# Kernel optimization log

Hardware: AMD Instinct MI355X
Metric: run time of the kernel (lower is better)

Reference implementation:

```python
import jax, jax.numpy as jnp
import numpy as np

M, IN_F, OUT_F = 16384, 2048, 2048

def sign_fn(x):
    # torch.sign(torch.sign(x) + 0.5): maps 0 -> +1, otherwise +/-1
    return jnp.sign(jnp.sign(x) + 0.5)

def setup_inputs() -> dict:
    key = jax.random.key(0)
    kx, kw = jax.random.split(key)
    # Upstream BNN activations are binary +/-1 (required for the packed-bit
    # backward in the original module to be exact).
    x = sign_fn(jax.random.normal(kx, (M, IN_F), dtype=jnp.float32))
    weight = jax.random.uniform(kw, (OUT_F, IN_F), dtype=jnp.float32) * 0.01
    return {"x": x, "weight": weight}

def reference(x, weight):
    # xnor=False path: SignFunctionNoSTE -> binarize weight, then dense matmul
    b_weight = sign_fn(weight)          # [OUT_F, IN_F], values in {-1, +1}
    return x @ b_weight.T               # [M, OUT_F]
```

## Files before the change

### kernel.cpp

```cpp
#include <hip/hip_runtime.h>
#include <stdint.h>

typedef unsigned long long u64;

#define M_DIM 16384
#define N_DIM 2048
#define K_DIM 2048

#define BM 256
#define BN 256
#define BK 64
#define NSTAGE (K_DIM / BK)

typedef int v4i  __attribute__((ext_vector_type(4)));
typedef int v16i __attribute__((ext_vector_type(16)));


__device__ __forceinline__ void gld16(void* lds_base, const void* gsrc) {
    __builtin_amdgcn_global_load_lds(
        (const __attribute__((address_space(1))) uint32_t*)gsrc,
        (__attribute__((address_space(3))) uint32_t*)lds_base,
        16, 0, 0);
}

__device__ __forceinline__ int pk4(float a, float b, float c, float d) {
    int r = (a < 0.0f ? 0xFF : 0x01);
    r |= (b < 0.0f ? 0xFF : 0x01) << 8;
    r |= (c < 0.0f ? 0xFF : 0x01) << 16;
    r |= (d < 0.0f ? 0xFF : 0x01) << 24;
    return r;
}

template <int T>
__global__ __launch_bounds__(256) void pack_i8_kernel(
        const float* __restrict__ src, char* __restrict__ dst) {
    const int wave_id = (blockIdx.x * 256 + threadIdx.x) >> 6;
    const int lane = threadIdx.x & 63;
    const int s  = wave_id & (NSTAGE - 1);
    const int rg = wave_id >> 5;
    const int r  = lane & 31;
    const int kh = lane >> 5;
    const int regs = 2 * T;
    char* out = dst + ((size_t)rg * NSTAGE + s) * (regs * 1024) + lane * 16;
#pragma unroll 2
    for (int rr = 0; rr < regs; ++rr) {
        const int c = rr / T, t = rr % T;
        const int row = rg * (T * 32) + t * 32 + r;
        const float* p = src + (size_t)row * K_DIM + s * BK + c * 32 + kh * 16;
        const float4 v0 = ((const float4*)p)[0];
        const float4 v1 = ((const float4*)p)[1];
        const float4 v2 = ((const float4*)p)[2];
        const float4 v3 = ((const float4*)p)[3];
        int4 o;
        o.x = pk4(v0.x, v0.y, v0.z, v0.w);
        o.y = pk4(v1.x, v1.y, v1.z, v1.w);
        o.z = pk4(v2.x, v2.y, v2.z, v2.w);
        o.w = pk4(v3.x, v3.y, v3.z, v3.w);
        *(int4*)(out + rr * 1024) = o;
    }
}

__global__ __launch_bounds__(512, 2) void bgemm_i8_kernel(
        const char* __restrict__ Ap, const char* __restrict__ Bp,
        float* __restrict__ C) {
    __shared__ __align__(16) char lds[2][32 * 1024];

    const int t    = threadIdx.x;
    const int lane = t & 63;
    const int wv   = t >> 6;
    const int wm   = (wv >> 1) & 3;
    const int wn   = wv & 1;

    const int id    = blockIdx.x;
    const int xcd   = id & 7;
    const int idx   = id >> 3;
    const int m_blk = xcd * 8 + (idx & 7);
    const int n_blk = idx >> 3;

    const char* aG = Ap + (size_t)m_blk * (NSTAGE * 16384);
    const char* bG = Bp + (size_t)n_blk * (NSTAGE * 16384);

    v16i acc[2][4];
#pragma unroll
    for (int i = 0; i < 2; ++i)
#pragma unroll
        for (int j = 0; j < 4; ++j)
#pragma unroll
            for (int q = 0; q < 16; ++q) acc[i][j][q] = 0;

    auto dma = [&](int s, int buf) {
        const char* a = aG + (size_t)s * 16384;
        const char* b = bG + (size_t)s * 16384;
#pragma unroll
        for (int r = 0; r < 4; ++r) {
            const int reg = wv * 4 + r;
            const char* g = (reg < 16) ? (a + reg * 1024)
                                       : (b + (reg - 16) * 1024);
            gld16(&lds[buf][reg * 1024], g + lane * 16);
        }
    };

    auto compute = [&](int buf) {
        const char* As = lds[buf];
        const char* Bs = lds[buf] + 16384;
#pragma unroll
        for (int c = 0; c < 2; ++c) {
            v4i af[2], bf[4];
#pragma unroll
            for (int i = 0; i < 2; ++i)
                af[i] = *(const v4i*)(As + (c * 8 + wm * 2 + i) * 1024 + lane * 16);
#pragma unroll
            for (int j = 0; j < 4; ++j)
                bf[j] = *(const v4i*)(Bs + (c * 8 + wn * 4 + j) * 1024 + lane * 16);
#pragma unroll
            for (int i = 0; i < 2; ++i)
#pragma unroll
                for (int j = 0; j < 4; ++j)
                    acc[i][j] = __builtin_amdgcn_mfma_i32_32x32x32_i8(
                        af[i], bf[j], acc[i][j], 0, 0, 0);
        }
    };

    dma(0, 0);
    __syncthreads();
#pragma unroll 1
    for (int s = 0; s < NSTAGE; ++s) {
        if (s + 1 < NSTAGE) dma(s + 1, (s + 1) & 1);
        compute(s & 1);
        __syncthreads();
    }

    const int col = lane & 31;
    const int rq  = (lane >> 5) * 4;
#pragma unroll
    for (int i = 0; i < 2; ++i) {
#pragma unroll
        for (int j = 0; j < 4; ++j) {
            const int mbase = m_blk * BM + (wm * 2 + i) * 32;
            const int nbase = n_blk * BN + (wn * 4 + j) * 32;
#pragma unroll
            for (int q = 0; q < 16; ++q) {
                const int row = mbase + (q & 3) + 8 * (q >> 2) + rq;
                C[(size_t)row * N_DIM + nbase + col] = (float)acc[i][j][q];
            }
        }
    }
}

#define KC 32
#define KT 16
struct alignas(16) u64x2 { u64 x, y; };

__global__ __launch_bounds__(256) void pack_sign_kernel(
        const float* __restrict__ in, u64* __restrict__ out, int ngroups) {
    int wid  = (blockIdx.x * 256 + threadIdx.x) >> 6;
    int lane = threadIdx.x & 63;
    if (wid >= ngroups) return;
    const float4* p = reinterpret_cast<const float4*>(in) + (size_t)wid * 64 + lane;
    float4 v = *p;
    u64 b0 = __ballot(v.x < 0.0f);
    u64 b1 = __ballot(v.y < 0.0f);
    u64 b2 = __ballot(v.z < 0.0f);
    u64 b3 = __ballot(v.w < 0.0f);
    if (lane == 0) {
        u64* o = out + (size_t)wid * 4;
        o[0] = b0; o[1] = b1; o[2] = b2; o[3] = b3;
    }
}

__global__ __launch_bounds__(256, 2) void bgemm_kernel(
        const u64* __restrict__ A, const u64* __restrict__ B,
        float* __restrict__ C) {
    __shared__ u64 As[KT][128];
    __shared__ u64 Bs[KT][128];
    const int t     = threadIdx.x;
    const int m_blk = blockIdx.y << 7;
    const int n_blk = blockIdx.x << 7;
    const int lane = t & 63;
    const int wave = t >> 6;
    const int tm   = lane >> 3;
    const int tn   = lane & 7;
    const int m0   = ((wave >> 1) << 6) + (tm << 3);
    const int n0   = ((wave & 1) << 6) + (tn << 3);
    unsigned acc[8][8];
#pragma unroll
    for (int i = 0; i < 8; ++i)
#pragma unroll
        for (int j = 0; j < 8; ++j) acc[i][j] = 0u;
    const int sr = t >> 3;
    const int sc = (t << 1) & 15;
    for (int ks = 0; ks < K_DIM / (KT * 64); ++ks) {
        const int cbase = ks * KT;
#pragma unroll
        for (int i = 0; i < 4; ++i) {
            int r = i * 32 + sr;
            u64x2 va = *reinterpret_cast<const u64x2*>(A + (size_t)(m_blk + r) * KC + cbase + sc);
            As[sc][r] = va.x; As[sc + 1][r] = va.y;
            u64x2 vb = *reinterpret_cast<const u64x2*>(B + (size_t)(n_blk + r) * KC + cbase + sc);
            Bs[sc][r] = vb.x; Bs[sc + 1][r] = vb.y;
        }
        __syncthreads();
#pragma unroll 1
        for (int c = 0; c < KT; ++c) {
            u64 a[8], b[8];
#pragma unroll
            for (int i = 0; i < 4; ++i) {
                u64x2 va = *reinterpret_cast<const u64x2*>(&As[c][m0 + 2 * i]);
                a[2 * i] = va.x; a[2 * i + 1] = va.y;
                u64x2 vb = *reinterpret_cast<const u64x2*>(&Bs[c][n0 + 2 * i]);
                b[2 * i] = vb.x; b[2 * i + 1] = vb.y;
            }
#pragma unroll
            for (int i = 0; i < 8; ++i)
#pragma unroll
                for (int j = 0; j < 8; ++j)
                    acc[i][j] += (unsigned)__builtin_popcountll(a[i] ^ b[j]);
        }
        __syncthreads();
    }
#pragma unroll
    for (int i = 0; i < 8; ++i) {
        float* o = C + (size_t)(m_blk + m0 + i) * N_DIM + n_blk + n0;
        float4 v0, v1;
        v0.x = (float)(K_DIM - 2 * (int)acc[i][0]);
        v0.y = (float)(K_DIM - 2 * (int)acc[i][1]);
        v0.z = (float)(K_DIM - 2 * (int)acc[i][2]);
        v0.w = (float)(K_DIM - 2 * (int)acc[i][3]);
        v1.x = (float)(K_DIM - 2 * (int)acc[i][4]);
        v1.y = (float)(K_DIM - 2 * (int)acc[i][5]);
        v1.z = (float)(K_DIM - 2 * (int)acc[i][6]);
        v1.w = (float)(K_DIM - 2 * (int)acc[i][7]);
        *reinterpret_cast<float4*>(o)     = v0;
        *reinterpret_cast<float4*>(o + 4) = v1;
    }
}

extern "C" void kernel_launch(void* const* d_in, const int* in_sizes, int n_in,
                              void* d_out, int out_size, void* d_ws, size_t ws_size,
                              hipStream_t stream) {
    const float* x = (const float*)d_in[0];
    const float* w = (const float*)d_in[1];
    float* out = (float*)d_out;

    const size_t needA = (size_t)M_DIM * K_DIM;
    const size_t needB = (size_t)N_DIM * K_DIM;
    if (ws_size >= needA + needB) {
        char* Ap = (char*)d_ws;
        char* Bp = Ap + needA;
        pack_i8_kernel<8><<<2048 / 4, 256, 0, stream>>>(x, Ap);
        pack_i8_kernel<8><<<256 / 4, 256, 0, stream>>>(w, Bp);
        bgemm_i8_kernel<<<(M_DIM / BM) * (N_DIM / BN), 512, 0, stream>>>(Ap, Bp, out);
    } else {
        u64* xb = (u64*)d_ws;
        u64* wb = xb + (size_t)M_DIM * KC;
        int xgroups = (M_DIM * K_DIM) / 256;
        int wgroups = (N_DIM * K_DIM) / 256;
        pack_sign_kernel<<<xgroups / 4, 256, 0, stream>>>(x, xb, xgroups);
        pack_sign_kernel<<<wgroups / 4, 256, 0, stream>>>(w, wb, wgroups);
        bgemm_kernel<<<dim3(N_DIM / 128, M_DIM / 128), 256, 0, stream>>>(xb, wb, out);
    }
}
```

Baseline: 318.8 us.

## Switch binary GEMM from int8 MFMA to FP4 scaled MFMA

Packs the ±1 values as FP4 (E2M1) nibbles (0x2 = +1, 0xA = -1) instead of int8 bytes, halving the packed operand size and the workspace. The GEMM now uses the gfx950 scaled f8f6f4 32x32x64 MFMA with FP4 format and unit scales, covering K=128 per stage and accumulating in fp32. This is meant to cut operand memory traffic and double the K consumed per MFMA. In exchange it depends on the FP4 register layout and operand zero-padding being correct. The fp32 accumulation stays exact because all sums are integers well below 2^24.

Measured after the change: 286.3 us. 10.2% less time.

```diff
diff --git a/kernel.cpp b/kernel.cpp
--- a/kernel.cpp
+++ b/kernel.cpp
@@ -7,14 +7,15 @@
 #define N_DIM 2048
 #define K_DIM 2048
 
+
 #define BM 256
 #define BN 256
-#define BK 64
-#define NSTAGE (K_DIM / BK)
-
-typedef int v4i  __attribute__((ext_vector_type(4)));
-typedef int v16i __attribute__((ext_vector_type(16)));
-
+#define BK 128
+#define NST (K_DIM / BK)
+
+typedef int   v4i  __attribute__((ext_vector_type(4)));
+typedef int   v8i  __attribute__((ext_vector_type(8)));
+typedef float v16f __attribute__((ext_vector_type(16)));
 
 __device__ __forceinline__ void gld16(void* lds_base, const void* gsrc) {
     __builtin_amdgcn_global_load_lds(
@@ -23,44 +24,46 @@
         16, 0, 0);
 }
 
-__device__ __forceinline__ int pk4(float a, float b, float c, float d) {
-    int r = (a < 0.0f ? 0xFF : 0x01);
-    r |= (b < 0.0f ? 0xFF : 0x01) << 8;
-    r |= (c < 0.0f ? 0xFF : 0x01) << 16;
-    r |= (d < 0.0f ? 0xFF : 0x01) << 24;
+__device__ __forceinline__ int pkn(float4 a, float4 b) {
+    int r;
+    r  = (a.x < 0.0f ? 0xA : 0x2);
+    r |= (a.y < 0.0f ? 0xA : 0x2) << 4;
+    r |= (a.z < 0.0f ? 0xA : 0x2) << 8;
+    r |= (a.w < 0.0f ? 0xA : 0x2) << 12;
+    r |= (b.x < 0.0f ? 0xA : 0x2) << 16;
+    r |= (b.y < 0.0f ? 0xA : 0x2) << 20;
+    r |= (b.z < 0.0f ? 0xA : 0x2) << 24;
+    r |= (b.w < 0.0f ? 0xA : 0x2) << 28;
     return r;
 }
 
-template <int T>
-__global__ __launch_bounds__(256) void pack_i8_kernel(
+__global__ __launch_bounds__(256) void pack_fp4_kernel(
         const float* __restrict__ src, char* __restrict__ dst) {
-    const int wave_id = (blockIdx.x * 256 + threadIdx.x) >> 6;
+    const int wid  = (blockIdx.x * 256 + threadIdx.x) >> 6;
     const int lane = threadIdx.x & 63;
-    const int s  = wave_id & (NSTAGE - 1);
-    const int rg = wave_id >> 5;
-    const int r  = lane & 31;
-    const int kh = lane >> 5;
-    const int regs = 2 * T;
-    char* out = dst + ((size_t)rg * NSTAGE + s) * (regs * 1024) + lane * 16;
-#pragma unroll 2
-    for (int rr = 0; rr < regs; ++rr) {
-        const int c = rr / T, t = rr % T;
-        const int row = rg * (T * 32) + t * 32 + r;
-        const float* p = src + (size_t)row * K_DIM + s * BK + c * 32 + kh * 16;
-        const float4 v0 = ((const float4*)p)[0];
-        const float4 v1 = ((const float4*)p)[1];
-        const float4 v2 = ((const float4*)p)[2];
-        const float4 v3 = ((const float4*)p)[3];
-        int4 o;
-        o.x = pk4(v0.x, v0.y, v0.z, v0.w);
-        o.y = pk4(v1.x, v1.y, v1.z, v1.w);
-        o.z = pk4(v2.x, v2.y, v2.z, v2.w);
-        o.w = pk4(v3.x, v3.y, v3.z, v3.w);
-        *(int4*)(out + rr * 1024) = o;
-    }
-}
-
-__global__ __launch_bounds__(512, 2) void bgemm_i8_kernel(
+    const int t    = wid & 7;
+    const int sub  = (wid >> 3) & 1;
+    const int st   = (wid >> 4) & 15;
+    const int blk  = wid >> 8;
+    const int row  = blk * 256 + t * 32 + (lane & 31);
+    const int kb   = st * 128 + sub * 64 + (lane >> 5) * 32;
+    const float4* p = (const float4*)(src + (size_t)row * K_DIM + kb);
+    int4 o;
+    o.x = pkn(p[0], p[1]);
+    o.y = pkn(p[2], p[3]);
+    o.z = pkn(p[4], p[5]);
+    o.w = pkn(p[6], p[7]);
+    *(int4*)(dst + (size_t)wid * 1024 + lane * 16) = o;
+}
+
+__device__ __forceinline__ v8i up8(v4i v) {
+    v8i r;
+    r[0] = v[0]; r[1] = v[1]; r[2] = v[2]; r[3] = v[3];
+    r[4] = 0;    r[5] = 0;    r[6] = 0;    r[7] = 0;
+    return r;
+}
+
+__global__ __launch_bounds__(512, 2) void bgemm_fp4_kernel(
         const char* __restrict__ Ap, const char* __restrict__ Bp,
         float* __restrict__ C) {
     __shared__ __align__(16) char lds[2][32 * 1024];
@@ -77,16 +80,16 @@
     const int m_blk = xcd * 8 + (idx & 7);
     const int n_blk = idx >> 3;
 
-    const char* aG = Ap + (size_t)m_blk * (NSTAGE * 16384);
-    const char* bG = Bp + (size_t)n_blk * (NSTAGE * 16384);
-
-    v16i acc[2][4];
+    const char* aG = Ap + (size_t)m_blk * (NST * 16384);
+    const char* bG = Bp + (size_t)n_blk * (NST * 16384);
+
+    v16f acc[2][4];
 #pragma unroll
     for (int i = 0; i < 2; ++i)
 #pragma unroll
         for (int j = 0; j < 4; ++j)
 #pragma unroll
-            for (int q = 0; q < 16; ++q) acc[i][j][q] = 0;
+            for (int q = 0; q < 16; ++q) acc[i][j][q] = 0.0f;
 
     auto dma = [&](int s, int buf) {
         const char* a = aG + (size_t)s * 16384;
@@ -104,28 +107,31 @@
         const char* As = lds[buf];
         const char* Bs = lds[buf] + 16384;
 #pragma unroll
-        for (int c = 0; c < 2; ++c) {
-            v4i af[2], bf[4];
+        for (int sub = 0; sub < 2; ++sub) {
+            v8i af[2], bf[4];
 #pragma unroll
             for (int i = 0; i < 2; ++i)
-                af[i] = *(const v4i*)(As + (c * 8 + wm * 2 + i) * 1024 + lane * 16);
+                af[i] = up8(*(const v4i*)(As + (sub * 8 + wm * 2 + i) * 1024 + lane * 16));
 #pragma unroll
             for (int j = 0; j < 4; ++j)
-                bf[j] = *(const v4i*)(Bs + (c * 8 + wn * 4 + j) * 1024 + lane * 16);
+                bf[j] = up8(*(const v4i*)(Bs + (sub * 8 + wn * 4 + j) * 1024 + lane * 16));
 #pragma unroll
             for (int i = 0; i < 2; ++i)
 #pragma unroll
                 for (int j = 0; j < 4; ++j)
-                    acc[i][j] = __builtin_amdgcn_mfma_i32_32x32x32_i8(
-                        af[i], bf[j], acc[i][j], 0, 0, 0);
+                    acc[i][j] = __builtin_amdgcn_mfma_scale_f32_32x32x64_f8f6f4(
+                        af[i], bf[j], acc[i][j],
+                        4, 4,
+                        0, 0x7F7F7F7F,
+                        0, 0x7F7F7F7F);
         }
     };
 
     dma(0, 0);
     __syncthreads();
 #pragma unroll 1
-    for (int s = 0; s < NSTAGE; ++s) {
-        if (s + 1 < NSTAGE) dma(s + 1, (s + 1) & 1);
+    for (int s = 0; s < NST; ++s) {
+        if (s + 1 < NST) dma(s + 1, (s + 1) & 1);
         compute(s & 1);
         __syncthreads();
     }
@@ -141,7 +147,7 @@
 #pragma unroll
             for (int q = 0; q < 16; ++q) {
                 const int row = mbase + (q & 3) + 8 * (q >> 2) + rq;
-                C[(size_t)row * N_DIM + nbase + col] = (float)acc[i][j][q];
+                C[(size_t)row * N_DIM + nbase + col] = acc[i][j][q];
             }
         }
     }
@@ -242,14 +248,14 @@
     const float* w = (const float*)d_in[1];
     float* out = (float*)d_out;
 
-    const size_t needA = (size_t)M_DIM * K_DIM;
-    const size_t needB = (size_t)N_DIM * K_DIM;
+    const size_t needA = (size_t)M_DIM * K_DIM / 2;
+    const size_t needB = (size_t)N_DIM * K_DIM / 2;
     if (ws_size >= needA + needB) {
         char* Ap = (char*)d_ws;
         char* Bp = Ap + needA;
-        pack_i8_kernel<8><<<2048 / 4, 256, 0, stream>>>(x, Ap);
-        pack_i8_kernel<8><<<256 / 4, 256, 0, stream>>>(w, Bp);
-        bgemm_i8_kernel<<<(M_DIM / BM) * (N_DIM / BN), 512, 0, stream>>>(Ap, Bp, out);
+        pack_fp4_kernel<<<4096, 256, 0, stream>>>(x, Ap);
+        pack_fp4_kernel<<<512, 256, 0, stream>>>(w, Bp);
+        bgemm_fp4_kernel<<<(M_DIM / BM) * (N_DIM / BN), 512, 0, stream>>>(Ap, Bp, out);
     } else {
         u64* xb = (u64*)d_ws;
         u64* wb = xb + (size_t)M_DIM * KC;
```
